# Kernel optimization log

Hardware: AMD Instinct MI355X
Metric: run time of the kernel (lower is better)

Reference implementation:

```python
import jax, jax.numpy as jnp
import numpy as np

B, S, D, DS, NSLOT = 2, 1024, 1024, 320, 512
H, CH = 4, 5
DFF = 4 * D
MAXIT = 2


def _ln(x, g, b, eps=1e-5):
    m = x.mean(-1, keepdims=True)
    v = ((x - m) ** 2).mean(-1, keepdims=True)
    return (x - m) * jax.lax.rsqrt(v + eps) * g + b


def _mha(x, Wq, Wk, Wv, Wo, bq, bk, bv, bo, nh):
    b_, s_, d_ = x.shape
    hd = d_ // nh
    q = (x @ Wq + bq).reshape(b_, s_, nh, hd)
    k = (x @ Wk + bk).reshape(b_, s_, nh, hd)
    v = (x @ Wv + bv).reshape(b_, s_, nh, hd)
    a = jax.nn.softmax(jnp.einsum('bqhd,bkhd->bhqk', q, k) * (hd ** -0.5), axis=-1)
    o = jnp.einsum('bhqk,bkhd->bqhd', a, v).reshape(b_, s_, d_)
    return o @ Wo + bo


def setup_inputs():
    key = jax.random.key(0)
    ks = iter(jax.random.split(key, 64))
    n = lambda shape: jax.random.normal(next(ks), shape, jnp.float32) * 0.02
    z = lambda shape: jnp.zeros(shape, jnp.float32)
    o = lambda shape: jnp.ones(shape, jnp.float32)
    return dict(
        x=jax.random.normal(next(ks), (B, S, D), jnp.float32),
        cache=jax.random.normal(next(ks), (B, NSLOT, DS), jnp.float32),
        iter_emb=n((16, D)),
        rq_w=n((D, D)), rg_w=n((D, 1)), rg_b=z((1,)), ck_w=n((DS, D)), cv_w=n((DS, D)),
        aq_w=n((D, D)), ak_w=n((D, D)), av_w=n((D, D)), ao_w=n((D, D)),
        aq_b=z((D,)), ak_b=z((D,)), av_b=z((D,)), ao_b=z((D,)),
        f1_w=n((D, DFF)), f1_b=z((DFF,)), f2_w=n((DFF, D)), f2_b=z((D,)),
        n1_g=o((D,)), n1_b=z((D,)), n2_g=o((D,)), n2_b=z((D,)),
        sq_w=n((DS, DS)), tk_w=n((D, DS)), tv_w=n((D, DS)), wg_w=n((D, 1)), wg_b=z((1,)),
        cq_w=n((DS, DS)), ck2_w=n((DS, DS)), cv2_w=n((DS, DS)), co_w=n((DS, DS)),
        cq_b=z((DS,)), ck2_b=z((DS,)), cv2_b=z((DS,)), co_b=z((DS,)),
        cn_g=o((DS,)), cn_b=z((DS,)),
        max_iterations=MAXIT,
    )


def reference(x, cache, iter_emb, rq_w, rg_w, rg_b, ck_w, cv_w,
              aq_w, ak_w, av_w, ao_w, aq_b, ak_b, av_b, ao_b,
              f1_w, f1_b, f2_w, f2_b, n1_g, n1_b, n2_g, n2_b,
              sq_w, tk_w, tv_w, wg_w, wg_b,
              cq_w, ck2_w, cv2_w, co_w, cq_b, ck2_b, cv2_b, co_b, cn_g, cn_b,
              max_iterations):
    def mem_read(h, cc):
        # gather from cache: gated cross-attention readout
        q = h @ rq_w                                   # [B,S,D]
        k = cc @ ck_w                                  # [B,N,D]
        v = cc @ cv_w                                  # [B,N,D]
        a = jax.nn.softmax(jnp.einsum('bsd,bnd->bsn', q, k) * (D ** -0.5), axis=-1)
        readout = jnp.einsum('bsn,bnd->bsd', a, v)
        gate = jax.nn.sigmoid(h @ rg_w + rg_b)          # [B,S,1] soft read gate
        return h + gate * readout

    def compute_block(h):
        # faithful to ComputeBlock (non-linear-attention branch): norm1 used twice
        hn = _ln(h, n1_g, n1_b)
        attn = _mha(hn, aq_w, ak_w, av_w, ao_w, aq_b, ak_b, av_b, ao_b, H)
        h = _ln(h + attn, n1_g, n1_b)
        ffn = jax.nn.gelu(h @ f1_w + f1_b) @ f2_w + f2_b
        return _ln(h + ffn, n2_g, n2_b)

    def mem_write(h, cc):
        # importance-scored scatter: slots attend over tokens, gated by importance
        sq = cc @ sq_w                                  # [B,N,DS]
        tk = h @ tk_w                                   # [B,S,DS]
        tv = h @ tv_w                                   # [B,S,DS]
        gate = jax.nn.sigmoid(h @ wg_w + wg_b)          # [B,S,1] soft write gate
        a = jax.nn.softmax(jnp.einsum('bnd,bsd->bns', sq, tk) * (DS ** -0.5), axis=-1)
        upd = jnp.einsum('bns,bsd->bnd', a, gate * tv)
        return cc + upd

    def cache_self_attn(cc):
        attn = _mha(cc, cq_w, ck2_w, cv2_w, co_w, cq_b, ck2_b, cv2_b, co_b, CH)
        return _ln(cc + attn, cn_g, cn_b)

    h = x
    cc = cache
    layer_input = x
    h_prev = None
    for it in range(max_iterations):
        h = h + iter_emb[it][None, None, :]
        if it > 0:
            h = h + layer_input + h_prev
        h_enh = mem_read(h, cc)
        h_comp = compute_block(h_enh)
        cc = mem_write(h_comp, cc)
        cc = cache_self_attn(cc)
        h = h_comp
        h_prev = jax.lax.stop_gradient(h_comp)  # torch: h_prev = h_computed.detach()
    return h
```

## Files before the change

kernel.cpp:

```cpp
#include <hip/hip_runtime.h>
#include <cstdint>

constexpr int B_ = 2, S_ = 1024, D_ = 1024, DS_ = 320, NSLOT_ = 512;
constexpr int H_ = 4, CH_ = 5, DFF_ = 4096;
constexpr int HD_ = D_ / H_;
constexpr int CHD_ = DS_ / CH_;
constexpr int BS_ = B_ * S_;
constexpr int BNS_ = B_ * NSLOT_;

typedef unsigned short u16;
typedef __attribute__((ext_vector_type(8))) short bf16x8;
typedef __attribute__((ext_vector_type(4))) float f32x4;
typedef __attribute__((ext_vector_type(4))) u16 u16x4;

__device__ __forceinline__ u16 f2bf(float f) {
  unsigned u = __float_as_uint(f);
  return (u16)((u + 0x7FFFu + ((u >> 16) & 1u)) >> 16);
}
__device__ __forceinline__ float bf2f(u16 h) { return __uint_as_float((unsigned)h << 16); }

__device__ __forceinline__ void gload16(const void* g, void* l) {
  __builtin_amdgcn_global_load_lds((const __attribute__((address_space(1))) void*)g,
                                   (__attribute__((address_space(3))) void*)l, 16, 0, 0);
}

template<int BN>
__global__ __launch_bounds__(512, 4)
void k_gemm(const u16* __restrict__ A, int lda, long long sA, long long sA2,
            const u16* __restrict__ Bp, int ldb, long long sB, long long sB2,
            float* __restrict__ outF, u16* __restrict__ outB,
            int ldc, long long sC, long long sC2,
            u16* __restrict__ outBT, int ldt, long long sT, long long sT2,
            int K, int zdiv, const float* __restrict__ bias,
            const float* __restrict__ rowscale, int act)
{
  constexpr int BM = 128;
  constexpr int MI = (BN == 128) ? 2 : 1;
  constexpr int NI = 4;
  constexpr int WROWS = MI * 16;
  constexpr int ABYT = BM * 128;
  constexpr int BBYT = BN * 128;
  constexpr int BUF = ABYT + BBYT;
  const int z = blockIdx.z, zb = z / zdiv, zr = z - zb * zdiv;
  A  += (long long)zb * sA + (long long)zr * sA2;
  Bp += (long long)zb * sB + (long long)zr * sB2;
  const long long cof = (long long)zb * sC + (long long)zr * sC2;
  const long long tof = (long long)zb * sT + (long long)zr * sT2;
  const int bm = blockIdx.y * BM, bn = blockIdx.x * BN;
  __shared__ __align__(16) char lds[2 * BUF];
  const int tid = threadIdx.x;
  const int lane = tid & 63, wid = tid >> 6;
  const int wm = (BN == 128) ? (wid >> 1) : wid;
  const int wn = (BN == 128) ? (wid & 1) : 0;
  const int rowb = wm * WROWS, colb = wn * 64;

  f32x4 acc[MI][NI];
  const f32x4 fz = {0.f, 0.f, 0.f, 0.f};
  #pragma unroll
  for (int i = 0; i < MI; ++i)
    #pragma unroll
    for (int j = 0; j < NI; ++j) acc[i][j] = fz;

  const int trow = tid >> 3;
  const int tg   = ((tid & 7) ^ (trow & 7)) * 8;
  const u16* gA  = A + (long long)(bm + trow) * lda + tg;
  const u16* gA2 = gA + (long long)64 * lda;
  const u16* gB  = Bp + (long long)(bn + trow) * ldb + tg;
  const u16* gB2 = gB + (long long)64 * ldb;

  auto stage = [&](int buf, int k0) {
    char* la = lds + buf * BUF + wid * 1024;
    char* lb = lds + buf * BUF + ABYT + wid * 1024;
    gload16(gA + k0, la);
    gload16(gA2 + k0, la + 8192);
    gload16(gB + k0, lb);
    if constexpr (BN == 128) gload16(gB2 + k0, lb + 8192);
  };

  const int r = lane & 15, q = lane >> 4;
  const int c7 = r & 7;
  const int gs0 = ((q) ^ c7) << 4;
  const int gs1 = ((4 + q) ^ c7) << 4;
  int aoff[MI], boff[NI];
  #pragma unroll
  for (int i = 0; i < MI; ++i) aoff[i] = (rowb + i * 16 + r) * 128;
  #pragma unroll
  for (int j = 0; j < NI; ++j) boff[j] = (colb + j * 16 + r) * 128;

  const int nsteps = K >> 6;
  stage(0, 0);
  int cur = 0;
  for (int it = 0; it < nsteps; ++it) {
    if (it + 1 < nsteps) {
      stage(cur ^ 1, (it + 1) << 6);
      if constexpr (BN == 128) asm volatile("s_waitcnt vmcnt(4)" ::: "memory");
      else                     asm volatile("s_waitcnt vmcnt(3)" ::: "memory");
    } else {
      asm volatile("s_waitcnt vmcnt(0)" ::: "memory");
    }
    __builtin_amdgcn_s_barrier();
    __builtin_amdgcn_sched_barrier(0);
    const char* pa = lds + cur * BUF;
    const char* pb = pa + ABYT;
    #pragma unroll
    for (int s = 0; s < 2; ++s) {
      const int gso = s ? gs1 : gs0;
      bf16x8 af[MI], bv[NI];
      #pragma unroll
      for (int i = 0; i < MI; ++i) af[i] = *(const bf16x8*)(pa + aoff[i] + gso);
      #pragma unroll
      for (int j = 0; j < NI; ++j) bv[j] = *(const bf16x8*)(pb + boff[j] + gso);
      #pragma unroll
      for (int i = 0; i < MI; ++i)
        #pragma unroll
        for (int j = 0; j < NI; ++j)
          acc[i][j] = __builtin_amdgcn_mfma_f32_16x16x32_bf16(af[i], bv[j], acc[i][j], 0, 0, 0);
    }
    asm volatile("s_waitcnt lgkmcnt(0)" ::: "memory");
    __builtin_amdgcn_sched_barrier(0);
    __builtin_amdgcn_s_barrier();
    cur ^= 1;
  }

  const int fr = lane & 15, fq = lane >> 4;
  #pragma unroll
  for (int i = 0; i < MI; ++i) {
    const int r0 = bm + rowb + i * 16 + fq * 4;
    #pragma unroll
    for (int j = 0; j < NI; ++j) {
      const int cn = bn + colb + j * 16 + fr;
      const float bvv = bias ? bias[cn] : 0.f;
      float vv[4];
      #pragma unroll
      for (int t = 0; t < 4; ++t) {
        float v = acc[i][j][t] + bvv;
        if (rowscale) v *= rowscale[r0 + t];
        if (act) v = 0.5f * v * (1.f + tanhf(0.7978845608028654f * (v + 0.044715f * v * v * v)));
        vv[t] = v;
      }
      if (outF) {
        #pragma unroll
        for (int t = 0; t < 4; ++t) outF[cof + (long long)(r0 + t) * ldc + cn] = vv[t];
      }
      if (outB) {
        #pragma unroll
        for (int t = 0; t < 4; ++t) outB[cof + (long long)(r0 + t) * ldc + cn] = f2bf(vv[t]);
      }
      if (outBT) {
        u16x4 pk = {f2bf(vv[0]), f2bf(vv[1]), f2bf(vv[2]), f2bf(vv[3])};
        *(u16x4*)(outBT + tof + (long long)cn * ldt + r0) = pk;
      }
    }
  }
}

__global__ __launch_bounds__(256)
void k_tcvt(const float* __restrict__ in, u16* __restrict__ out, int R, int C)
{
  __shared__ float t[32][33];
  const int bx = blockIdx.x * 32, by = blockIdx.y * 32;
  const int tx = threadIdx.x & 31, ty = threadIdx.x >> 5;
  #pragma unroll
  for (int i = 0; i < 32; i += 8)
    t[ty + i][tx] = in[(long long)(by + ty + i) * C + bx + tx];
  __syncthreads();
  #pragma unroll
  for (int i = 0; i < 32; i += 8)
    out[(long long)(bx + ty + i) * R + by + tx] = f2bf(t[tx][ty + i]);
}

__global__ __launch_bounds__(256)
void k_cvt(const float* __restrict__ in, u16* __restrict__ out, int n)
{
  int i = blockIdx.x * 256 + threadIdx.x;
  if (i < n) out[i] = f2bf(in[i]);
}

__global__ __launch_bounds__(256)
void k_softmax_b16(u16* __restrict__ x, int cols, float scale)
{
  u16* p = x + (long long)blockIdx.x * cols;
  const int tid = threadIdx.x;
  __shared__ float red[256];
  float v[4];
  float m = -1e30f;
  #pragma unroll
  for (int i = 0; i < 4; ++i) {
    const int c = tid + (i << 8);
    v[i] = (c < cols) ? bf2f(p[c]) * scale : -1e30f;
    m = fmaxf(m, v[i]);
  }
  red[tid] = m; __syncthreads();
  for (int s = 128; s > 0; s >>= 1) { if (tid < s) red[tid] = fmaxf(red[tid], red[tid + s]); __syncthreads(); }
  m = red[0]; __syncthreads();
  float sum = 0.f;
  #pragma unroll
  for (int i = 0; i < 4; ++i) { v[i] = expf(v[i] - m); sum += v[i]; }
  red[tid] = sum; __syncthreads();
  for (int s = 128; s > 0; s >>= 1) { if (tid < s) red[tid] += red[tid + s]; __syncthreads(); }
  const float inv = 1.f / red[0];
  #pragma unroll
  for (int i = 0; i < 4; ++i) {
    const int c = tid + (i << 8);
    if (c < cols) p[c] = f2bf(v[i] * inv);
  }
}

__global__ __launch_bounds__(256)
void k_layernorm(const float* __restrict__ x, const float* __restrict__ res,
                 const float* __restrict__ g, const float* __restrict__ b,
                 float* __restrict__ outF, u16* __restrict__ outB, int cols)
{
  const long long ro = (long long)blockIdx.x * cols;
  const float* px = x + ro;
  const float* pr = res ? res + ro : nullptr;
  __shared__ float red[256];
  const int tid = threadIdx.x;
  float s = 0.f;
  for (int c = tid; c < cols; c += 256) { float v = px[c] + (pr ? pr[c] : 0.f); s += v; }
  red[tid] = s; __syncthreads();
  for (int t = 128; t > 0; t >>= 1) { if (tid < t) red[tid] += red[tid + t]; __syncthreads(); }
  const float mean = red[0] / cols; __syncthreads();
  float s2 = 0.f;
  for (int c = tid; c < cols; c += 256) { float v = px[c] + (pr ? pr[c] : 0.f) - mean; s2 += v * v; }
  red[tid] = s2; __syncthreads();
  for (int t = 128; t > 0; t >>= 1) { if (tid < t) red[tid] += red[tid + t]; __syncthreads(); }
  const float inv = rsqrtf(red[0] / cols + 1e-5f);
  for (int c = tid; c < cols; c += 256) {
    float v = (px[c] + (pr ? pr[c] : 0.f) - mean) * inv * g[c] + b[c];
    if (outF) outF[ro + c] = v;
    if (outB) outB[ro + c] = f2bf(v);
  }
}

__global__ __launch_bounds__(256)
void k_gate(const float* __restrict__ x, const float* __restrict__ w,
            const float* __restrict__ b0, float* __restrict__ out, int cols)
{
  const int lane = threadIdx.x & 63;
  const int wv = threadIdx.x >> 6;
  const long long row = (long long)blockIdx.x * 4 + wv;
  const float* p = x + row * cols;
  float s = 0.f;
  for (int c = lane; c < cols; c += 64) s += p[c] * w[c];
  #pragma unroll
  for (int off = 32; off > 0; off >>= 1) s += __shfl_down(s, off);
  if (lane == 0) out[row] = 1.0f / (1.0f + expf(-(s + b0[0])));
}

__global__ __launch_bounds__(256)
void k_combine2(float* __restrict__ oF, u16* __restrict__ oB,
                const float* __restrict__ a, float sa, const float* __restrict__ b,
                const float* __restrict__ emb, int n, int Dm1)
{
  int i = blockIdx.x * 256 + threadIdx.x;
  if (i >= n) return;
  float v = sa * a[i];
  if (b) v += b[i];
  v += emb[i & Dm1];
  oF[i] = v; oB[i] = f2bf(v);
}

__global__ __launch_bounds__(256)
void k_gated_add(float* __restrict__ out, const float* __restrict__ h,
                 const float* __restrict__ r, const float* __restrict__ gate, int n, int Dv)
{
  int i = blockIdx.x * 256 + threadIdx.x;
  if (i >= n) return;
  out[i] = h[i] + gate[i / Dv] * r[i];
}

__global__ __launch_bounds__(256)
void k_add2(float* __restrict__ oF, u16* __restrict__ oB,
            const float* __restrict__ a, const float* __restrict__ b, int n)
{
  int i = blockIdx.x * 256 + threadIdx.x;
  if (i >= n) return;
  float v = a[i] + b[i];
  oF[i] = v; oB[i] = f2bf(v);
}

extern "C" void kernel_launch(void* const* d_in, const int* in_sizes, int n_in,
                              void* d_out, int out_size, void* d_ws, size_t ws_size,
                              hipStream_t stream)
{
  (void)in_sizes; (void)n_in; (void)out_size;
  const float* x        = (const float*)d_in[0];
  const float* cache0   = (const float*)d_in[1];
  const float* iter_emb = (const float*)d_in[2];
  const float* rq_w     = (const float*)d_in[3];
  const float* rg_w     = (const float*)d_in[4];
  const float* rg_b     = (const float*)d_in[5];
  const float* ck_w     = (const float*)d_in[6];
  const float* cv_w     = (const float*)d_in[7];
  const float* aq_w     = (const float*)d_in[8];
  const float* ak_w     = (const float*)d_in[9];
  const float* av_w     = (const float*)d_in[10];
  const float* ao_w     = (const float*)d_in[11];
  const float* aq_b     = (const float*)d_in[12];
  const float* ak_b     = (const float*)d_in[13];
  const float* av_b     = (const float*)d_in[14];
  const float* ao_b     = (const float*)d_in[15];
  const float* f1_w     = (const float*)d_in[16];
  const float* f1_b     = (const float*)d_in[17];
  const float* f2_w     = (const float*)d_in[18];
  const float* f2_b     = (const float*)d_in[19];
  const float* n1_g     = (const float*)d_in[20];
  const float* n1_b     = (const float*)d_in[21];
  const float* n2_g     = (const float*)d_in[22];
  const float* n2_b     = (const float*)d_in[23];
  const float* sq_w     = (const float*)d_in[24];
  const float* tk_w     = (const float*)d_in[25];
  const float* tv_w     = (const float*)d_in[26];
  const float* wg_w     = (const float*)d_in[27];
  const float* wg_b     = (const float*)d_in[28];
  const float* cq_w     = (const float*)d_in[29];
  const float* ck2_w    = (const float*)d_in[30];
  const float* cv2_w    = (const float*)d_in[31];
  const float* co_w     = (const float*)d_in[32];
  const float* cq_b     = (const float*)d_in[33];
  const float* ck2_b    = (const float*)d_in[34];
  const float* cv2_b    = (const float*)d_in[35];
  const float* co_b     = (const float*)d_in[36];
  const float* cn_g     = (const float*)d_in[37];
  const float* cn_b     = (const float*)d_in[38];

  float* out = (float*)d_out;

  size_t off = 0;
  char* base = (char*)d_ws;
  auto allocF = [&](size_t n) { float* p = (float*)(base + off); off += n * 4; off = (off + 255) & ~(size_t)255; return p; };
  auto allocH = [&](size_t n) { u16* p = (u16*)(base + off); off += n * 2; off = (off + 255) & ~(size_t)255; return p; };

  float* hbuf  = allocF((size_t)BS_ * D_);
  float* henh  = allocF((size_t)BS_ * D_);
  float* hcomp = allocF((size_t)BS_ * D_);
  float* h2b   = allocF((size_t)BS_ * D_);
  float* tA    = allocF((size_t)BS_ * D_);
  float* gate  = allocF((size_t)BS_);
  float* ccnf  = allocF((size_t)BNS_ * DS_);
  float* updf  = allocF((size_t)BNS_ * DS_);
  float* coo   = allocF((size_t)BNS_ * DS_);
  float* ccwf  = allocF((size_t)BNS_ * DS_);
  u16* rqT  = allocH((size_t)D_ * D_);
  u16* ckT  = allocH((size_t)D_ * DS_);
  u16* cvT  = allocH((size_t)D_ * DS_);
  u16* aqT  = allocH((size_t)D_ * D_);
  u16* akT  = allocH((size_t)D_ * D_);
  u16* avT  = allocH((size_t)D_ * D_);
  u16* aoT  = allocH((size_t)D_ * D_);
  u16* f1T  = allocH((size_t)DFF_ * D_);
  u16* f2T  = allocH((size_t)D_ * DFF_);
  u16* sqT  = allocH((size_t)DS_ * DS_);
  u16* tkT  = allocH((size_t)DS_ * D_);
  u16* tvTw = allocH((size_t)DS_ * D_);
  u16* cqT  = allocH((size_t)DS_ * DS_);
  u16* ck2T = allocH((size_t)DS_ * DS_);
  u16* cv2T = allocH((size_t)DS_ * DS_);
  u16* coT  = allocH((size_t)DS_ * DS_);
  u16* bb1  = allocH((size_t)BS_ * D_);
  u16* bb2  = allocH((size_t)BS_ * D_);
  u16* bb3  = allocH((size_t)BS_ * D_);
  u16* bb4  = allocH((size_t)BS_ * D_);
  u16* bb5  = allocH((size_t)B_ * H_ * S_ * S_);
  u16* cc0b = allocH((size_t)BNS_ * DS_);
  u16* ccwb = allocH((size_t)BNS_ * DS_);
  u16* sqb  = allocH((size_t)BNS_ * DS_);
  u16* tkb  = allocH((size_t)BS_ * DS_);
  u16* tvTb = allocH((size_t)DS_ * BS_);
  u16* ccnb = allocH((size_t)BNS_ * DS_);
  u16* cqb  = allocH((size_t)BNS_ * DS_);
  u16* ck2b = allocH((size_t)BNS_ * DS_);
  u16* cv2Tb= allocH((size_t)DS_ * BNS_);
  u16* csab = allocH((size_t)BNS_ * DS_);
  if (off > ws_size) return;

  auto gemm = [&](int M, int N, int K, int z, int zdiv,
                  const u16* Ap, int lda, long long sa, long long sa2,
                  const u16* Bq, int ldb, long long sb, long long sb2,
                  float* oF, u16* oB, int ldc, long long sc, long long sc2,
                  u16* oBT, int ldt, long long st, long long st2,
                  const float* bias, const float* rsc, int act) {
    const long long blocks128 = (N % 128 == 0) ? (long long)(N / 128) * (M / 128) * z : 0;
    if (N % 128 == 0 && blocks128 >= 256) {
      dim3 g(N / 128, M / 128, z);
      k_gemm<128><<<g, 512, 0, stream>>>(Ap, lda, sa, sa2, Bq, ldb, sb, sb2,
          oF, oB, ldc, sc, sc2, oBT, ldt, st, st2, K, zdiv, bias, rsc, act);
    } else {
      dim3 g(N / 64, M / 128, z);
      k_gemm<64><<<g, 512, 0, stream>>>(Ap, lda, sa, sa2, Bq, ldb, sb, sb2,
          oF, oB, ldc, sc, sc2, oBT, ldt, st, st2, K, zdiv, bias, rsc, act);
    }
  };
  auto tcvt = [&](const float* in, u16* o, int R, int C) {
    dim3 g(C / 32, R / 32);
    k_tcvt<<<g, 256, 0, stream>>>(in, o, R, C);
  };
  auto lnorm = [&](const float* xp, const float* rp, const float* g, const float* b,
                   float* oF, u16* oB, int rows, int cols) {
    k_layernorm<<<rows, 256, 0, stream>>>(xp, rp, g, b, oF, oB, cols);
  };
  auto eg = [](int n) { return dim3((n + 255) / 256); };

  tcvt(rq_w, rqT, D_, D_);
  tcvt(ck_w, ckT, DS_, D_);
  tcvt(cv_w, cvT, DS_, D_);
  tcvt(aq_w, aqT, D_, D_);
  tcvt(ak_w, akT, D_, D_);
  tcvt(av_w, avT, D_, D_);
  tcvt(ao_w, aoT, D_, D_);
  tcvt(f1_w, f1T, D_, DFF_);
  tcvt(f2_w, f2T, DFF_, D_);
  tcvt(sq_w, sqT, DS_, DS_);
  tcvt(tk_w, tkT, D_, DS_);
  tcvt(tv_w, tvTw, D_, DS_);
  tcvt(cq_w, cqT, DS_, DS_);
  tcvt(ck2_w, ck2T, DS_, DS_);
  tcvt(cv2_w, cv2T, DS_, DS_);
  tcvt(co_w, coT, DS_, DS_);
  k_cvt<<<eg(BNS_ * DS_), 256, 0, stream>>>(cache0, cc0b, BNS_ * DS_);

  auto mem_read = [&](const float* h_f, const u16* h_b, const u16* cc_b, float* o_henh) {
    gemm(BS_, D_, D_, 1, 1, h_b, D_, 0, 0, rqT, D_, 0, 0,
         nullptr, bb2, D_, 0, 0, nullptr, 0, 0, 0, nullptr, nullptr, 0);
    gemm(BNS_, D_, DS_, 1, 1, cc_b, DS_, 0, 0, ckT, DS_, 0, 0,
         nullptr, bb3, D_, 0, 0, nullptr, 0, 0, 0, nullptr, nullptr, 0);
    gemm(BNS_, D_, DS_, 1, 1, cc_b, DS_, 0, 0, cvT, DS_, 0, 0,
         nullptr, nullptr, 0, 0, 0, bb4, BNS_, 0, 0, nullptr, nullptr, 0);
    gemm(S_, NSLOT_, D_, B_, 1, bb2, D_, (long long)S_ * D_, 0,
         bb3, D_, (long long)NSLOT_ * D_, 0,
         nullptr, bb5, NSLOT_, (long long)S_ * NSLOT_, 0,
         nullptr, 0, 0, 0, nullptr, nullptr, 0);
    k_softmax_b16<<<B_ * S_, 256, 0, stream>>>(bb5, NSLOT_, 0.03125f);
    gemm(S_, D_, NSLOT_, B_, 1, bb5, NSLOT_, (long long)S_ * NSLOT_, 0,
         bb4, BNS_, NSLOT_, 0,
         tA, nullptr, D_, (long long)S_ * D_, 0,
         nullptr, 0, 0, 0, nullptr, nullptr, 0);
    k_gate<<<BS_ / 4, 256, 0, stream>>>(h_f, rg_w, rg_b, gate, D_);
    k_gated_add<<<eg(BS_ * D_), 256, 0, stream>>>(o_henh, h_f, tA, gate, BS_ * D_, D_);
  };

  auto compute_block = [&](const float* he, float* oF, u16* oB) {
    lnorm(he, nullptr, n1_g, n1_b, nullptr, bb1, BS_, D_);
    gemm(BS_, D_, D_, 1, 1, bb1, D_, 0, 0, aqT, D_, 0, 0,
         nullptr, bb2, D_, 0, 0, nullptr, 0, 0, 0, aq_b, nullptr, 0);
    gemm(BS_, D_, D_, 1, 1, bb1, D_, 0, 0, akT, D_, 0, 0,
         nullptr, bb3, D_, 0, 0, nullptr, 0, 0, 0, ak_b, nullptr, 0);
    gemm(BS_, D_, D_, 1, 1, bb1, D_, 0, 0, avT, D_, 0, 0,
         nullptr, nullptr, 0, 0, 0, bb4, BS_, 0, 0, av_b, nullptr, 0);
    gemm(S_, S_, HD_, B_ * H_, H_,
         bb2, D_, (long long)S_ * D_, HD_,
         bb3, D_, (long long)S_ * D_, HD_,
         nullptr, bb5, S_, (long long)H_ * S_ * S_, (long long)S_ * S_,
         nullptr, 0, 0, 0, nullptr, nullptr, 0);
    k_softmax_b16<<<B_ * H_ * S_, 256, 0, stream>>>(bb5, S_, 0.0625f);
    gemm(S_, HD_, S_, B_ * H_, H_,
         bb5, S_, (long long)H_ * S_ * S_, (long long)S_ * S_,
         bb4, BS_, S_, (long long)HD_ * BS_,
         nullptr, bb2, D_, (long long)S_ * D_, HD_,
         nullptr, 0, 0, 0, nullptr, nullptr, 0);
    gemm(BS_, D_, D_, 1, 1, bb2, D_, 0, 0, aoT, D_, 0, 0,
         tA, nullptr, D_, 0, 0, nullptr, 0, 0, 0, ao_b, nullptr, 0);
    lnorm(he, tA, n1_g, n1_b, h2b, bb1, BS_, D_);
    gemm(BS_, DFF_, D_, 1, 1, bb1, D_, 0, 0, f1T, D_, 0, 0,
         nullptr, bb5, DFF_, 0, 0, nullptr, 0, 0, 0, f1_b, nullptr, 1);
    gemm(BS_, D_, DFF_, 1, 1, bb5, DFF_, 0, 0, f2T, DFF_, 0, 0,
         tA, nullptr, D_, 0, 0, nullptr, 0, 0, 0, f2_b, nullptr, 0);
    lnorm(h2b, tA, n2_g, n2_b, oF, oB, BS_, D_);
  };

  auto mem_write_csa = [&](const float* hc_f, const u16* hc_b,
                           const float* ccin_f, const u16* ccin_b) {
    gemm(BNS_, DS_, DS_, 1, 1, ccin_b, DS_, 0, 0, sqT, DS_, 0, 0,
         nullptr, sqb, DS_, 0, 0, nullptr, 0, 0, 0, nullptr, nullptr, 0);
    gemm(BS_, DS_, D_, 1, 1, hc_b, D_, 0, 0, tkT, D_, 0, 0,
         nullptr, tkb, DS_, 0, 0, nullptr, 0, 0, 0, nullptr, nullptr, 0);
    k_gate<<<BS_ / 4, 256, 0, stream>>>(hc_f, wg_w, wg_b, gate, D_);
    gemm(BS_, DS_, D_, 1, 1, hc_b, D_, 0, 0, tvTw, D_, 0, 0,
         nullptr, nullptr, 0, 0, 0, tvTb, BS_, 0, 0, nullptr, gate, 0);
    gemm(NSLOT_, S_, DS_, B_, 1, sqb, DS_, (long long)NSLOT_ * DS_, 0,
         tkb, DS_, (long long)S_ * DS_, 0,
         nullptr, bb5, S_, (long long)NSLOT_ * S_, 0,
         nullptr, 0, 0, 0, nullptr, nullptr, 0);
    k_softmax_b16<<<B_ * NSLOT_, 256, 0, stream>>>(bb5, S_, 0.05590169943749474f);
    gemm(NSLOT_, DS_, S_, B_, 1, bb5, S_, (long long)NSLOT_ * S_, 0,
         tvTb, BS_, S_, 0,
         updf, nullptr, DS_, (long long)NSLOT_ * DS_, 0,
         nullptr, 0, 0, 0, nullptr, nullptr, 0);
    k_add2<<<eg(BNS_ * DS_), 256, 0, stream>>>(ccnf, ccnb, ccin_f, updf, BNS_ * DS_);
    gemm(BNS_, DS_, DS_, 1, 1, ccnb, DS_, 0, 0, cqT, DS_, 0, 0,
         nullptr, cqb, DS_, 0, 0, nullptr, 0, 0, 0, cq_b, nullptr, 0);
    gemm(BNS_, DS_, DS_, 1, 1, ccnb, DS_, 0, 0, ck2T, DS_, 0, 0,
         nullptr, ck2b, DS_, 0, 0, nullptr, 0, 0, 0, ck2_b, nullptr, 0);
    gemm(BNS_, DS_, DS_, 1, 1, ccnb, DS_, 0, 0, cv2T, DS_, 0, 0,
         nullptr, nullptr, 0, 0, 0, cv2Tb, BNS_, 0, 0, cv2_b, nullptr, 0);
    gemm(NSLOT_, NSLOT_, CHD_, B_ * CH_, CH_,
         cqb, DS_, (long long)NSLOT_ * DS_, CHD_,
         ck2b, DS_, (long long)NSLOT_ * DS_, CHD_,
         nullptr, bb5, NSLOT_, (long long)CH_ * NSLOT_ * NSLOT_, (long long)NSLOT_ * NSLOT_,
         nullptr, 0, 0, 0, nullptr, nullptr, 0);
    k_softmax_b16<<<B_ * CH_ * NSLOT_, 256, 0, stream>>>(bb5, NSLOT_, 0.125f);
    gemm(NSLOT_, CHD_, NSLOT_, B_ * CH_, CH_,
         bb5, NSLOT_, (long long)CH_ * NSLOT_ * NSLOT_, (long long)NSLOT_ * NSLOT_,
         cv2Tb, BNS_, NSLOT_, (long long)CHD_ * BNS_,
         nullptr, csab, DS_, (long long)NSLOT_ * DS_, CHD_,
         nullptr, 0, 0, 0, nullptr, nullptr, 0);
    gemm(BNS_, DS_, DS_, 1, 1, csab, DS_, 0, 0, coT, DS_, 0, 0,
         coo, nullptr, DS_, 0, 0, nullptr, 0, 0, 0, co_b, nullptr, 0);
    lnorm(ccnf, coo, cn_g, cn_b, ccwf, ccwb, BNS_, DS_);
  };

  k_combine2<<<eg(BS_ * D_), 256, 0, stream>>>(hbuf, bb1, x, 1.0f, nullptr, iter_emb, BS_ * D_, D_ - 1);
  mem_read(hbuf, bb1, cc0b, henh);
  compute_block(henh, hcomp, bb3);
  mem_write_csa(hcomp, bb3, cache0, cc0b);

  k_combine2<<<eg(BS_ * D_), 256, 0, stream>>>(hbuf, bb1, hcomp, 2.0f, x, iter_emb + D_, BS_ * D_, D_ - 1);
  mem_read(hbuf, bb1, ccwb, henh);
  compute_block(henh, out, nullptr);
}
```

Baseline: 625.0 us.

## Fuse QKV and paired projections into single GEMMs, split-K the FFN down-projection

Merges the separate Q/K/V projection GEMMs, the ck/cv and tk/tv GEMMs, and the cache QKV GEMMs into single wider GEMMs. A new split-column epilogue sends the leading columns to a row-major output and the rest to a transposed output, and a column threshold controls where the row scale applies. The FFN second GEMM now splits K in two, and the extra partial sum plus the bias are added inside the following layernorm. The fusions assume the transposed weight buffers sit next to each other in the workspace. The aim is fewer launches and enough blocks to fill the GPU, at the cost of an extra fp32 partial buffer and a changed rule for choosing tile size.

```diff
diff --git a/kernel.cpp b/kernel.cpp
--- a/kernel.cpp
+++ b/kernel.cpp
@@ -12,6 +12,7 @@
 typedef __attribute__((ext_vector_type(8))) short bf16x8;
 typedef __attribute__((ext_vector_type(4))) float f32x4;
 typedef __attribute__((ext_vector_type(4))) u16 u16x4;
+typedef long long ll;
 
 __device__ __forceinline__ u16 f2bf(float f) {
   unsigned u = __float_as_uint(f);
@@ -26,13 +27,14 @@
 
 template<int BN>
 __global__ __launch_bounds__(512, 4)
-void k_gemm(const u16* __restrict__ A, int lda, long long sA, long long sA2,
-            const u16* __restrict__ Bp, int ldb, long long sB, long long sB2,
+void k_gemm(const u16* __restrict__ A, int lda, ll sA, ll sA2,
+            const u16* __restrict__ Bp, int ldb, ll sB, ll sB2,
             float* __restrict__ outF, u16* __restrict__ outB,
-            int ldc, long long sC, long long sC2,
-            u16* __restrict__ outBT, int ldt, long long sT, long long sT2,
+            int ldc, ll sC, ll sC2,
+            u16* __restrict__ outBT, int ldt, ll sT, ll sT2,
             int K, int zdiv, const float* __restrict__ bias,
-            const float* __restrict__ rowscale, int act)
+            const float* __restrict__ rowscale, int rscfrom,
+            int splitcol, int act)
 {
   constexpr int BM = 128;
   constexpr int MI = (BN == 128) ? 2 : 1;
@@ -42,10 +44,10 @@
   constexpr int BBYT = BN * 128;
   constexpr int BUF = ABYT + BBYT;
   const int z = blockIdx.z, zb = z / zdiv, zr = z - zb * zdiv;
-  A  += (long long)zb * sA + (long long)zr * sA2;
-  Bp += (long long)zb * sB + (long long)zr * sB2;
-  const long long cof = (long long)zb * sC + (long long)zr * sC2;
-  const long long tof = (long long)zb * sT + (long long)zr * sT2;
+  A  += (ll)zb * sA + (ll)zr * sA2;
+  Bp += (ll)zb * sB + (ll)zr * sB2;
+  const ll cof = (ll)zb * sC + (ll)zr * sC2;
+  const ll tof = (ll)zb * sT + (ll)zr * sT2;
   const int bm = blockIdx.y * BM, bn = blockIdx.x * BN;
   __shared__ __align__(16) char lds[2 * BUF];
   const int tid = threadIdx.x;
@@ -63,19 +65,10 @@
 
   const int trow = tid >> 3;
   const int tg   = ((tid & 7) ^ (trow & 7)) * 8;
-  const u16* gA  = A + (long long)(bm + trow) * lda + tg;
-  const u16* gA2 = gA + (long long)64 * lda;
-  const u16* gB  = Bp + (long long)(bn + trow) * ldb + tg;
-  const u16* gB2 = gB + (long long)64 * ldb;
-
-  auto stage = [&](int buf, int k0) {
-    char* la = lds + buf * BUF + wid * 1024;
-    char* lb = lds + buf * BUF + ABYT + wid * 1024;
-    gload16(gA + k0, la);
-    gload16(gA2 + k0, la + 8192);
-    gload16(gB + k0, lb);
-    if constexpr (BN == 128) gload16(gB2 + k0, lb + 8192);
-  };
+  const u16* gA  = A + (ll)(bm + trow) * lda + tg;
+  const u16* gA2 = gA + (ll)64 * lda;
+  const u16* gB  = Bp + (ll)(bn + trow) * ldb + tg;
+  const u16* gB2 = gB + (ll)64 * ldb;
 
   const int r = lane & 15, q = lane >> 4;
   const int c7 = r & 7;
@@ -87,12 +80,22 @@
   #pragma unroll
   for (int j = 0; j < NI; ++j) boff[j] = (colb + j * 16 + r) * 128;
 
+  auto stage = [&](int buf, int it) {
+    char* la = lds + buf * BUF + wid * 1024;
+    char* lb = la + ABYT;
+    const int ko = it << 6;
+    gload16(gA + ko, la);
+    gload16(gA2 + ko, la + 8192);
+    gload16(gB + ko, lb);
+    if constexpr (BN == 128) gload16(gB2 + ko, lb + 8192);
+  };
+
   const int nsteps = K >> 6;
   stage(0, 0);
-  int cur = 0;
+  int bufp = 0;
   for (int it = 0; it < nsteps; ++it) {
     if (it + 1 < nsteps) {
-      stage(cur ^ 1, (it + 1) << 6);
+      stage(bufp ^ 1, it + 1);
       if constexpr (BN == 128) asm volatile("s_waitcnt vmcnt(4)" ::: "memory");
       else                     asm volatile("s_waitcnt vmcnt(3)" ::: "memory");
     } else {
@@ -100,7 +103,7 @@
     }
     __builtin_amdgcn_s_barrier();
     __builtin_amdgcn_sched_barrier(0);
-    const char* pa = lds + cur * BUF;
+    const char* pa = lds + bufp * BUF;
     const char* pb = pa + ABYT;
     #pragma unroll
     for (int s = 0; s < 2; ++s) {
@@ -119,7 +122,7 @@
     asm volatile("s_waitcnt lgkmcnt(0)" ::: "memory");
     __builtin_amdgcn_sched_barrier(0);
     __builtin_amdgcn_s_barrier();
-    cur ^= 1;
+    bufp ^= 1;
   }
 
   const int fr = lane & 15, fq = lane >> 4;
@@ -130,25 +133,27 @@
     for (int j = 0; j < NI; ++j) {
       const int cn = bn + colb + j * 16 + fr;
       const float bvv = bias ? bias[cn] : 0.f;
+      const bool doRs = rowscale && (cn >= rscfrom);
       float vv[4];
       #pragma unroll
       for (int t = 0; t < 4; ++t) {
         float v = acc[i][j][t] + bvv;
-        if (rowscale) v *= rowscale[r0 + t];
+        if (doRs) v *= rowscale[r0 + t];
         if (act) v = 0.5f * v * (1.f + tanhf(0.7978845608028654f * (v + 0.044715f * v * v * v)));
         vv[t] = v;
       }
-      if (outF) {
-        #pragma unroll
-        for (int t = 0; t < 4; ++t) outF[cof + (long long)(r0 + t) * ldc + cn] = vv[t];
-      }
-      if (outB) {
-        #pragma unroll
-        for (int t = 0; t < 4; ++t) outB[cof + (long long)(r0 + t) * ldc + cn] = f2bf(vv[t]);
-      }
-      if (outBT) {
+      if (cn < splitcol) {
+        if (outF) {
+          #pragma unroll
+          for (int t = 0; t < 4; ++t) outF[cof + (ll)(r0 + t) * ldc + cn] = vv[t];
+        }
+        if (outB) {
+          #pragma unroll
+          for (int t = 0; t < 4; ++t) outB[cof + (ll)(r0 + t) * ldc + cn] = f2bf(vv[t]);
+        }
+      } else {
         u16x4 pk = {f2bf(vv[0]), f2bf(vv[1]), f2bf(vv[2]), f2bf(vv[3])};
-        *(u16x4*)(outBT + tof + (long long)cn * ldt + r0) = pk;
+        *(u16x4*)(outBT + tof + (ll)(cn - splitcol) * ldt + r0) = pk;
       }
     }
   }
@@ -162,11 +167,11 @@
   const int tx = threadIdx.x & 31, ty = threadIdx.x >> 5;
   #pragma unroll
   for (int i = 0; i < 32; i += 8)
-    t[ty + i][tx] = in[(long long)(by + ty + i) * C + bx + tx];
+    t[ty + i][tx] = in[(ll)(by + ty + i) * C + bx + tx];
   __syncthreads();
   #pragma unroll
   for (int i = 0; i < 32; i += 8)
-    out[(long long)(bx + ty + i) * R + by + tx] = f2bf(t[tx][ty + i]);
+    out[(ll)(bx + ty + i) * R + by + tx] = f2bf(t[tx][ty + i]);
 }
 
 __global__ __launch_bounds__(256)
@@ -177,9 +182,19 @@
 }
 
 __global__ __launch_bounds__(256)
+void k_cat3f(float* __restrict__ dst, const float* __restrict__ a, int na,
+             const float* __restrict__ b, int nb, const float* __restrict__ c, int nc)
+{
+  int i = blockIdx.x * 256 + threadIdx.x;
+  if (i < na) dst[i] = a[i];
+  else if (i < na + nb) dst[i] = b[i - na];
+  else if (i < na + nb + nc) dst[i] = c[i - na - nb];
+}
+
+__global__ __launch_bounds__(256)
 void k_softmax_b16(u16* __restrict__ x, int cols, float scale)
 {
-  u16* p = x + (long long)blockIdx.x * cols;
+  u16* p = x + (ll)blockIdx.x * cols;
   const int tid = threadIdx.x;
   __shared__ float red[256];
   float v[4];
@@ -208,26 +223,35 @@
 
 __global__ __launch_bounds__(256)
 void k_layernorm(const float* __restrict__ x, const float* __restrict__ res,
+                 const float* __restrict__ res2, const float* __restrict__ rbias,
                  const float* __restrict__ g, const float* __restrict__ b,
                  float* __restrict__ outF, u16* __restrict__ outB, int cols)
 {
-  const long long ro = (long long)blockIdx.x * cols;
+  const ll ro = (ll)blockIdx.x * cols;
   const float* px = x + ro;
   const float* pr = res ? res + ro : nullptr;
+  const float* p2 = res2 ? res2 + ro : nullptr;
   __shared__ float red[256];
   const int tid = threadIdx.x;
+  auto val = [&](int c) {
+    float v = px[c];
+    if (pr) v += pr[c];
+    if (p2) v += p2[c];
+    if (rbias) v += rbias[c];
+    return v;
+  };
   float s = 0.f;
-  for (int c = tid; c < cols; c += 256) { float v = px[c] + (pr ? pr[c] : 0.f); s += v; }
+  for (int c = tid; c < cols; c += 256) s += val(c);
   red[tid] = s; __syncthreads();
   for (int t = 128; t > 0; t >>= 1) { if (tid < t) red[tid] += red[tid + t]; __syncthreads(); }
   const float mean = red[0] / cols; __syncthreads();
   float s2 = 0.f;
-  for (int c = tid; c < cols; c += 256) { float v = px[c] + (pr ? pr[c] : 0.f) - mean; s2 += v * v; }
+  for (int c = tid; c < cols; c += 256) { float v = val(c) - mean; s2 += v * v; }
   red[tid] = s2; __syncthreads();
   for (int t = 128; t > 0; t >>= 1) { if (tid < t) red[tid] += red[tid + t]; __syncthreads(); }
   const float inv = rsqrtf(red[0] / cols + 1e-5f);
   for (int c = tid; c < cols; c += 256) {
-    float v = (px[c] + (pr ? pr[c] : 0.f) - mean) * inv * g[c] + b[c];
+    float v = (val(c) - mean) * inv * g[c] + b[c];
     if (outF) outF[ro + c] = v;
     if (outB) outB[ro + c] = f2bf(v);
   }
@@ -239,7 +263,7 @@
 {
   const int lane = threadIdx.x & 63;
   const int wv = threadIdx.x >> 6;
-  const long long row = (long long)blockIdx.x * 4 + wv;
+  const ll row = (ll)blockIdx.x * 4 + wv;
   const float* p = x + row * cols;
   float s = 0.f;
   for (int c = lane; c < cols; c += 64) s += p[c] * w[c];
@@ -336,12 +360,14 @@
   float* henh  = allocF((size_t)BS_ * D_);
   float* hcomp = allocF((size_t)BS_ * D_);
   float* h2b   = allocF((size_t)BS_ * D_);
-  float* tA    = allocF((size_t)BS_ * D_);
+  float* tA    = allocF((size_t)2 * BS_ * D_);
   float* gate  = allocF((size_t)BS_);
   float* ccnf  = allocF((size_t)BNS_ * DS_);
   float* updf  = allocF((size_t)BNS_ * DS_);
   float* coo   = allocF((size_t)BNS_ * DS_);
   float* ccwf  = allocF((size_t)BNS_ * DS_);
+  float* qkvb  = allocF(3 * D_);
+  float* cqkvb = allocF(3 * DS_);
   u16* rqT  = allocH((size_t)D_ * D_);
   u16* ckT  = allocH((size_t)D_ * DS_);
   u16* cvT  = allocH((size_t)D_ * DS_);
@@ -363,42 +389,44 @@
   u16* bb3  = allocH((size_t)BS_ * D_);
   u16* bb4  = allocH((size_t)BS_ * D_);
   u16* bb5  = allocH((size_t)B_ * H_ * S_ * S_);
+  u16* bbQK = allocH((size_t)BS_ * 2 * D_);
+  u16* bbCQK= allocH((size_t)BNS_ * 2 * DS_);
   u16* cc0b = allocH((size_t)BNS_ * DS_);
   u16* ccwb = allocH((size_t)BNS_ * DS_);
   u16* sqb  = allocH((size_t)BNS_ * DS_);
   u16* tkb  = allocH((size_t)BS_ * DS_);
   u16* tvTb = allocH((size_t)DS_ * BS_);
   u16* ccnb = allocH((size_t)BNS_ * DS_);
-  u16* cqb  = allocH((size_t)BNS_ * DS_);
-  u16* ck2b = allocH((size_t)BNS_ * DS_);
   u16* cv2Tb= allocH((size_t)DS_ * BNS_);
   u16* csab = allocH((size_t)BNS_ * DS_);
   if (off > ws_size) return;
+  (void)cvT; (void)akT; (void)avT; (void)tvTw; (void)ck2T; (void)cv2T;
 
   auto gemm = [&](int M, int N, int K, int z, int zdiv,
-                  const u16* Ap, int lda, long long sa, long long sa2,
-                  const u16* Bq, int ldb, long long sb, long long sb2,
-                  float* oF, u16* oB, int ldc, long long sc, long long sc2,
-                  u16* oBT, int ldt, long long st, long long st2,
-                  const float* bias, const float* rsc, int act) {
-    const long long blocks128 = (N % 128 == 0) ? (long long)(N / 128) * (M / 128) * z : 0;
-    if (N % 128 == 0 && blocks128 >= 256) {
+                  const u16* Ap, int lda, ll sa, ll sa2,
+                  const u16* Bq, int ldb, ll sb, ll sb2,
+                  float* oF, u16* oB, int ldc, ll sc, ll sc2,
+                  u16* oBT, int ldt, ll st, ll st2,
+                  const float* bias, const float* rsc, int rscfrom,
+                  int splitcol, int act) {
+    const ll b64 = (ll)(N / 64) * (M / 128) * z;
+    if (N % 128 == 0 && b64 > 768 && (splitcol % 128) == 0) {
       dim3 g(N / 128, M / 128, z);
       k_gemm<128><<<g, 512, 0, stream>>>(Ap, lda, sa, sa2, Bq, ldb, sb, sb2,
-          oF, oB, ldc, sc, sc2, oBT, ldt, st, st2, K, zdiv, bias, rsc, act);
+          oF, oB, ldc, sc, sc2, oBT, ldt, st, st2, K, zdiv, bias, rsc, rscfrom, splitcol, act);
     } else {
       dim3 g(N / 64, M / 128, z);
       k_gemm<64><<<g, 512, 0, stream>>>(Ap, lda, sa, sa2, Bq, ldb, sb, sb2,
-          oF, oB, ldc, sc, sc2, oBT, ldt, st, st2, K, zdiv, bias, rsc, act);
+          oF, oB, ldc, sc, sc2, oBT, ldt, st, st2, K, zdiv, bias, rsc, rscfrom, splitcol, act);
     }
   };
   auto tcvt = [&](const float* in, u16* o, int R, int C) {
     dim3 g(C / 32, R / 32);
     k_tcvt<<<g, 256, 0, stream>>>(in, o, R, C);
   };
-  auto lnorm = [&](const float* xp, const float* rp, const float* g, const float* b,
-                   float* oF, u16* oB, int rows, int cols) {
-    k_layernorm<<<rows, 256, 0, stream>>>(xp, rp, g, b, oF, oB, cols);
+  auto lnorm = [&](const float* xp, const float* rp, const float* rp2, const float* rb,
+                   const float* g, const float* b, float* oF, u16* oB, int rows, int cols) {
+    k_layernorm<<<rows, 256, 0, stream>>>(xp, rp, rp2, rb, g, b, oF, oB, cols);
   };
   auto eg = [](int n) { return dim3((n + 255) / 256); };
 
@@ -419,95 +447,95 @@
   tcvt(cv2_w, cv2T, DS_, DS_);
   tcvt(co_w, coT, DS_, DS_);
   k_cvt<<<eg(BNS_ * DS_), 256, 0, stream>>>(cache0, cc0b, BNS_ * DS_);
+  k_cat3f<<<eg(3 * D_), 256, 0, stream>>>(qkvb, aq_b, D_, ak_b, D_, av_b, D_);
+  k_cat3f<<<eg(3 * DS_), 256, 0, stream>>>(cqkvb, cq_b, DS_, ck2_b, DS_, cv2_b, DS_);
 
   auto mem_read = [&](const float* h_f, const u16* h_b, const u16* cc_b, float* o_henh) {
     gemm(BS_, D_, D_, 1, 1, h_b, D_, 0, 0, rqT, D_, 0, 0,
-         nullptr, bb2, D_, 0, 0, nullptr, 0, 0, 0, nullptr, nullptr, 0);
-    gemm(BNS_, D_, DS_, 1, 1, cc_b, DS_, 0, 0, ckT, DS_, 0, 0,
-         nullptr, bb3, D_, 0, 0, nullptr, 0, 0, 0, nullptr, nullptr, 0);
-    gemm(BNS_, D_, DS_, 1, 1, cc_b, DS_, 0, 0, cvT, DS_, 0, 0,
-         nullptr, nullptr, 0, 0, 0, bb4, BNS_, 0, 0, nullptr, nullptr, 0);
-    gemm(S_, NSLOT_, D_, B_, 1, bb2, D_, (long long)S_ * D_, 0,
-         bb3, D_, (long long)NSLOT_ * D_, 0,
-         nullptr, bb5, NSLOT_, (long long)S_ * NSLOT_, 0,
-         nullptr, 0, 0, 0, nullptr, nullptr, 0);
+         nullptr, bb2, D_, 0, 0, nullptr, 0, 0, 0,
+         nullptr, nullptr, 0, D_, 0);
+    gemm(BNS_, 2 * D_, DS_, 1, 1, cc_b, DS_, 0, 0, ckT, DS_, 0, 0,
+         nullptr, bb3, D_, 0, 0, bb4, BNS_, 0, 0,
+         nullptr, nullptr, 0, D_, 0);
+    gemm(S_, NSLOT_, D_, B_, 1, bb2, D_, (ll)S_ * D_, 0,
+         bb3, D_, (ll)NSLOT_ * D_, 0,
+         nullptr, bb5, NSLOT_, (ll)S_ * NSLOT_, 0, nullptr, 0, 0, 0,
+         nullptr, nullptr, 0, NSLOT_, 0);
     k_softmax_b16<<<B_ * S_, 256, 0, stream>>>(bb5, NSLOT_, 0.03125f);
-    gemm(S_, D_, NSLOT_, B_, 1, bb5, NSLOT_, (long long)S_ * NSLOT_, 0,
+    gemm(S_, D_, NSLOT_, B_, 1, bb5, NSLOT_, (ll)S_ * NSLOT_, 0,
          bb4, BNS_, NSLOT_, 0,
-         tA, nullptr, D_, (long long)S_ * D_, 0,
-         nullptr, 0, 0, 0, nullptr, nullptr, 0);
+         tA, nullptr, D_, (ll)S_ * D_, 0, nullptr, 0, 0, 0,
+         nullptr, nullptr, 0, D_, 0);
     k_gate<<<BS_ / 4, 256, 0, stream>>>(h_f, rg_w, rg_b, gate, D_);
     k_gated_add<<<eg(BS_ * D_), 256, 0, stream>>>(o_henh, h_f, tA, gate, BS_ * D_, D_);
   };
 
   auto compute_block = [&](const float* he, float* oF, u16* oB) {
-    lnorm(he, nullptr, n1_g, n1_b, nullptr, bb1, BS_, D_);
-    gemm(BS_, D_, D_, 1, 1, bb1, D_, 0, 0, aqT, D_, 0, 0,
-         nullptr, bb2, D_, 0, 0, nullptr, 0, 0, 0, aq_b, nullptr, 0);
-    gemm(BS_, D_, D_, 1, 1, bb1, D_, 0, 0, akT, D_, 0, 0,
-         nullptr, bb3, D_, 0, 0, nullptr, 0, 0, 0, ak_b, nullptr, 0);
-    gemm(BS_, D_, D_, 1, 1, bb1, D_, 0, 0, avT, D_, 0, 0,
-         nullptr, nullptr, 0, 0, 0, bb4, BS_, 0, 0, av_b, nullptr, 0);
+    lnorm(he, nullptr, nullptr, nullptr, n1_g, n1_b, nullptr, bb1, BS_, D_);
+    gemm(BS_, 3 * D_, D_, 1, 1, bb1, D_, 0, 0, aqT, D_, 0, 0,
+         nullptr, bbQK, 2 * D_, 0, 0, bb4, BS_, 0, 0,
+         qkvb, nullptr, 0, 2 * D_, 0);
     gemm(S_, S_, HD_, B_ * H_, H_,
-         bb2, D_, (long long)S_ * D_, HD_,
-         bb3, D_, (long long)S_ * D_, HD_,
-         nullptr, bb5, S_, (long long)H_ * S_ * S_, (long long)S_ * S_,
-         nullptr, 0, 0, 0, nullptr, nullptr, 0);
+         bbQK, 2 * D_, (ll)S_ * 2 * D_, HD_,
+         bbQK + D_, 2 * D_, (ll)S_ * 2 * D_, HD_,
+         nullptr, bb5, S_, (ll)H_ * S_ * S_, (ll)S_ * S_, nullptr, 0, 0, 0,
+         nullptr, nullptr, 0, S_, 0);
     k_softmax_b16<<<B_ * H_ * S_, 256, 0, stream>>>(bb5, S_, 0.0625f);
     gemm(S_, HD_, S_, B_ * H_, H_,
-         bb5, S_, (long long)H_ * S_ * S_, (long long)S_ * S_,
-         bb4, BS_, S_, (long long)HD_ * BS_,
-         nullptr, bb2, D_, (long long)S_ * D_, HD_,
-         nullptr, 0, 0, 0, nullptr, nullptr, 0);
+         bb5, S_, (ll)H_ * S_ * S_, (ll)S_ * S_,
+         bb4, BS_, S_, (ll)HD_ * BS_,
+         nullptr, bb2, D_, (ll)S_ * D_, HD_, nullptr, 0, 0, 0,
+         nullptr, nullptr, 0, HD_, 0);
     gemm(BS_, D_, D_, 1, 1, bb2, D_, 0, 0, aoT, D_, 0, 0,
-         tA, nullptr, D_, 0, 0, nullptr, 0, 0, 0, ao_b, nullptr, 0);
-    lnorm(he, tA, n1_g, n1_b, h2b, bb1, BS_, D_);
+         tA, nullptr, D_, 0, 0, nullptr, 0, 0, 0,
+         ao_b, nullptr, 0, D_, 0);
+    lnorm(he, tA, nullptr, nullptr, n1_g, n1_b, h2b, bb1, BS_, D_);
     gemm(BS_, DFF_, D_, 1, 1, bb1, D_, 0, 0, f1T, D_, 0, 0,
-         nullptr, bb5, DFF_, 0, 0, nullptr, 0, 0, 0, f1_b, nullptr, 1);
-    gemm(BS_, D_, DFF_, 1, 1, bb5, DFF_, 0, 0, f2T, DFF_, 0, 0,
-         tA, nullptr, D_, 0, 0, nullptr, 0, 0, 0, f2_b, nullptr, 0);
-    lnorm(h2b, tA, n2_g, n2_b, oF, oB, BS_, D_);
+         nullptr, bb5, DFF_, 0, 0, nullptr, 0, 0, 0,
+         f1_b, nullptr, 0, DFF_, 1);
+    gemm(BS_, D_, 2048, 2, 2, bb5, DFF_, 0, 2048, f2T, DFF_, 0, 2048,
+         tA, nullptr, D_, 0, (ll)BS_ * D_, nullptr, 0, 0, 0,
+         nullptr, nullptr, 0, D_, 0);
+    lnorm(h2b, tA, tA + (ll)BS_ * D_, f2_b, n2_g, n2_b, oF, oB, BS_, D_);
   };
 
   auto mem_write_csa = [&](const float* hc_f, const u16* hc_b,
                            const float* ccin_f, const u16* ccin_b) {
     gemm(BNS_, DS_, DS_, 1, 1, ccin_b, DS_, 0, 0, sqT, DS_, 0, 0,
-         nullptr, sqb, DS_, 0, 0, nullptr, 0, 0, 0, nullptr, nullptr, 0);
-    gemm(BS_, DS_, D_, 1, 1, hc_b, D_, 0, 0, tkT, D_, 0, 0,
-         nullptr, tkb, DS_, 0, 0, nullptr, 0, 0, 0, nullptr, nullptr, 0);
+         nullptr, sqb, DS_, 0, 0, nullptr, 0, 0, 0,
+         nullptr, nullptr, 0, DS_, 0);
     k_gate<<<BS_ / 4, 256, 0, stream>>>(hc_f, wg_w, wg_b, gate, D_);
-    gemm(BS_, DS_, D_, 1, 1, hc_b, D_, 0, 0, tvTw, D_, 0, 0,
-         nullptr, nullptr, 0, 0, 0, tvTb, BS_, 0, 0, nullptr, gate, 0);
-    gemm(NSLOT_, S_, DS_, B_, 1, sqb, DS_, (long long)NSLOT_ * DS_, 0,
-         tkb, DS_, (long long)S_ * DS_, 0,
-         nullptr, bb5, S_, (long long)NSLOT_ * S_, 0,
-         nullptr, 0, 0, 0, nullptr, nullptr, 0);
+    gemm(BS_, 2 * DS_, D_, 1, 1, hc_b, D_, 0, 0, tkT, D_, 0, 0,
+         nullptr, tkb, DS_, 0, 0, tvTb, BS_, 0, 0,
+         nullptr, gate, DS_, DS_, 0);
+    gemm(NSLOT_, S_, DS_, B_, 1, sqb, DS_, (ll)NSLOT_ * DS_, 0,
+         tkb, DS_, (ll)S_ * DS_, 0,
+         nullptr, bb5, S_, (ll)NSLOT_ * S_, 0, nullptr, 0, 0, 0,
+         nullptr, nullptr, 0, S_, 0);
     k_softmax_b16<<<B_ * NSLOT_, 256, 0, stream>>>(bb5, S_, 0.05590169943749474f);
-    gemm(NSLOT_, DS_, S_, B_, 1, bb5, S_, (long long)NSLOT_ * S_, 0,
+    gemm(NSLOT_, DS_, S_, B_, 1, bb5, S_, (ll)NSLOT_ * S_, 0,
          tvTb, BS_, S_, 0,
-         updf, nullptr, DS_, (long long)NSLOT_ * DS_, 0,
-         nullptr, 0, 0, 0, nullptr, nullptr, 0);
+         updf, nullptr, DS_, (ll)NSLOT_ * DS_, 0, nullptr, 0, 0, 0,
+         nullptr, nullptr, 0, DS_, 0);
     k_add2<<<eg(BNS_ * DS_), 256, 0, stream>>>(ccnf, ccnb, ccin_f, updf, BNS_ * DS_);
-    gemm(BNS_, DS_, DS_, 1, 1, ccnb, DS_, 0, 0, cqT, DS_, 0, 0,
-         nullptr, cqb, DS_, 0, 0, nullptr, 0, 0, 0, cq_b, nullptr, 0);
-    gemm(BNS_, DS_, DS_, 1, 1, ccnb, DS_, 0, 0, ck2T, DS_, 0, 0,
-         nullptr, ck2b, DS_, 0, 0, nullptr, 0, 0, 0, ck2_b, nullptr, 0);
-    gemm(BNS_, DS_, DS_, 1, 1, ccnb, DS_, 0, 0, cv2T, DS_, 0, 0,
-         nullptr, nullptr, 0, 0, 0, cv2Tb, BNS_, 0, 0, cv2_b, nullptr, 0);
+    gemm(BNS_, 3 * DS_, DS_, 1, 1, ccnb, DS_, 0, 0, cqT, DS_, 0, 0,
+         nullptr, bbCQK, 2 * DS_, 0, 0, cv2Tb, BNS_, 0, 0,
+         cqkvb, nullptr, 0, 2 * DS_, 0);
     gemm(NSLOT_, NSLOT_, CHD_, B_ * CH_, CH_,
-         cqb, DS_, (long long)NSLOT_ * DS_, CHD_,
-         ck2b, DS_, (long long)NSLOT_ * DS_, CHD_,
-         nullptr, bb5, NSLOT_, (long long)CH_ * NSLOT_ * NSLOT_, (long long)NSLOT_ * NSLOT_,
-         nullptr, 0, 0, 0, nullptr, nullptr, 0);
+         bbCQK, 2 * DS_, (ll)NSLOT_ * 2 * DS_, CHD_,
+         bbCQK + DS_, 2 * DS_, (ll)NSLOT_ * 2 * DS_, CHD_,
+         nullptr, bb5, NSLOT_, (ll)CH_ * NSLOT_ * NSLOT_, (ll)NSLOT_ * NSLOT_,
+         nullptr, 0, 0, 0, nullptr, nullptr, 0, NSLOT_, 0);
     k_softmax_b16<<<B_ * CH_ * NSLOT_, 256, 0, stream>>>(bb5, NSLOT_, 0.125f);
     gemm(NSLOT_, CHD_, NSLOT_, B_ * CH_, CH_,
-         bb5, NSLOT_, (long long)CH_ * NSLOT_ * NSLOT_, (long long)NSLOT_ * NSLOT_,
-         cv2Tb, BNS_, NSLOT_, (long long)CHD_ * BNS_,
-         nullptr, csab, DS_, (long long)NSLOT_ * DS_, CHD_,
-         nullptr, 0, 0, 0, nullptr, nullptr, 0);
+         bb5, NSLOT_, (ll)CH_ * NSLOT_ * NSLOT_, (ll)NSLOT_ * NSLOT_,
+         cv2Tb, BNS_, NSLOT_, (ll)CHD_ * BNS_,
+         nullptr, csab, DS_, (ll)NSLOT_ * DS_, CHD_, nullptr, 0, 0, 0,
+         nullptr, nullptr, 0, CHD_, 0);
     gemm(BNS_, DS_, DS_, 1, 1, csab, DS_, 0, 0, coT, DS_, 0, 0,
-         coo, nullptr, DS_, 0, 0, nullptr, 0, 0, 0, co_b, nullptr, 0);
-    lnorm(ccnf, coo, cn_g, cn_b, ccwf, ccwb, BNS_, DS_);
+         coo, nullptr, DS_, 0, 0, nullptr, 0, 0, 0,
+         co_b, nullptr, 0, DS_, 0);
+    lnorm(ccnf, coo, nullptr, nullptr, cn_g, cn_b, ccwf, ccwb, BNS_, DS_);
   };
 
   k_combine2<<<eg(BS_ * D_), 256, 0, stream>>>(hbuf, bb1, x, 1.0f, nullptr, iter_emb, BS_ * D_, D_ - 1);
```

After: 578.3 us. 1.08x faster.
